# Optimization experiments

Hardware: AMD Instinct MI355X
Metric: run time of the kernel (lower is better)

## Reference

```python
import jax, jax.numpy as jnp
import numpy as np

LMDA = 1.0
SMOOTH = 1e-05

# 13 directional offsets (dz, dy, dx) matching the original slice pairs 1..13
OFFSETS = [
    (1, 0, 0), (0, 1, 0), (0, 0, 1),
    (1, 1, 0), (1, -1, 0),
    (0, 1, 1), (0, 1, -1),
    (1, 0, -1), (1, 0, 1),
    (1, -1, -1), (1, 1, -1),
    (-1, -1, -1), (-1, 1, -1),
]


def _shifted_diff(x, off):
    """x[..., pos-shift] - x[..., neg-shift] for offset off over last 3 dims."""
    sl_pos = tuple(slice(1, None) if o == 1 else (slice(None, -1) if o == -1 else slice(None)) for o in off)
    sl_neg = tuple(slice(None, -1) if o == 1 else (slice(1, None) if o == -1 else slice(None)) for o in off)
    return x[(Ellipsis,) + sl_pos] - x[(Ellipsis,) + sl_neg]


def setup_inputs() -> dict:
    key = jax.random.key(0)
    k1, k2 = jax.random.split(key)
    shape = (4, 1, 128, 192, 192)
    eps = 1e-6
    inp = jax.random.uniform(k1, shape, dtype=jnp.float32, minval=eps, maxval=1.0 - eps)
    tgt = jax.random.uniform(k2, shape, dtype=jnp.float32, minval=0.0, maxval=1.0)
    return {"input": inp, "target": tgt}


def reference(input, target):
    # region term: BCE with mean reduction
    bce = -jnp.mean(target * jnp.log(input) + (1.0 - target) * jnp.log(1.0 - input))

    # boundary term: 13 directional diff-product ratios
    acc = jnp.float32(0.0)
    for off in OFFSETS:
        di = _shifted_diff(input, off)
        dt = _shifted_diff(target, off)
        acc = acc + jnp.sum(di * dt) / (jnp.sum(dt * dt) + SMOOTH)
    boundary = 1.0 - acc / 13.0

    return LMDA * bce + boundary
```

## Files before the change

### kernel.cpp

```cpp
#include <hip/hip_runtime.h>
#include <math.h>

#define DX 192
#define DY 192
#define DZ 128
#define DB 4
#define DXY (DX*DY)
#define NTOT (DB*DZ*DXY)
#define XV (DX/4)
#define NCOL (DB*DZ*XV)
#define SEG 12
#define NSEG (DY/SEG)


__device__ inline float wred(float v) {
    #pragma unroll
    for (int o = 32; o > 0; o >>= 1) v += __shfl_down(v, o, 64);
    return v;
}

__device__ inline float4 ld4(const float* p) { return *(const float4*)p; }

#define TN(k, A1, A0, D1, D0) do { float di_=(A1)-(A0); float dt_=(D1)-(D0); \
    sk[k] += di_*dt_; rk[k] += dt_*dt_; } while(0)
#define TM(k, A1, A0, D1, D0) do { float di_=(A1)-(A0); float dt_=(D1)-(D0); \
    float dm_=fx3*dt_; sk[k] += di_*dm_; rk[k] += dt_*dm_; } while(0)
#define BCEACC(A0, D0) do { bces += (D0)*__logf(A0) + (1.0f-(D0))*__logf(1.0f-(A0)); } while(0)


#define ELEM_FULL(a0,a1,a2,a3,a4,a5,a6,a7, d0,d1,d2,d3,d4,d5,d6,d7) do { \
    TN(0,a4,a0,d4,d0); TN(1,a2,a0,d2,d0); TN(2,a1,a0,d1,d0); TN(3,a6,a0,d6,d0); \
    TN(4,a4,a2,d4,d2); TN(5,a3,a0,d3,d0); TN(6,a2,a1,d2,d1); TN(7,a4,a1,d4,d1); \
    TN(8,a5,a0,d5,d0); TN(9,a4,a3,d4,d3); TN(10,a6,a1,d6,d1); TN(11,a7,a0,d7,d0); \
    TN(12,a5,a2,d5,d2); BCEACC(a0,d0); } while(0)

#define ELEM_FX(a0,a1,a2,a3,a4,a5,a6,a7, d0,d1,d2,d3,d4,d5,d6,d7) do { \
    TN(0,a4,a0,d4,d0); TN(1,a2,a0,d2,d0); TM(2,a1,a0,d1,d0); TN(3,a6,a0,d6,d0); \
    TN(4,a4,a2,d4,d2); TM(5,a3,a0,d3,d0); TM(6,a2,a1,d2,d1); TM(7,a4,a1,d4,d1); \
    TM(8,a5,a0,d5,d0); TM(9,a4,a3,d4,d3); TM(10,a6,a1,d6,d1); TM(11,a7,a0,d7,d0); \
    TM(12,a5,a2,d5,d2); BCEACC(a0,d0); } while(0)

#define PEL_FULL(a0,a1,a4,a5, d0,d1,d4,d5) do { \
    TN(0,a4,a0,d4,d0); TN(2,a1,a0,d1,d0); TN(7,a4,a1,d4,d1); TN(8,a5,a0,d5,d0); \
    BCEACC(a0,d0); } while(0)
#define PEL_FX(a0,a1,a4,a5, d0,d1,d4,d5) do { \
    TN(0,a4,a0,d4,d0); TM(2,a1,a0,d1,d0); TM(7,a4,a1,d4,d1); TM(8,a5,a0,d5,d0); \
    BCEACC(a0,d0); } while(0)

#define ZEL_FULL(a0,a1,a2,a3, d0,d1,d2,d3) do { \
    TN(1,a2,a0,d2,d0); TN(2,a1,a0,d1,d0); TN(5,a3,a0,d3,d0); TN(6,a2,a1,d2,d1); \
    BCEACC(a0,d0); } while(0)
#define ZEL_FX(a0,a1,a2,a3, d0,d1,d2,d3) do { \
    TN(1,a2,a0,d2,d0); TM(2,a1,a0,d1,d0); TM(5,a3,a0,d3,d0); TM(6,a2,a1,d2,d1); \
    BCEACC(a0,d0); } while(0)

#define ZPEL_FULL(a0,a1, d0,d1) do { TN(2,a1,a0,d1,d0); BCEACC(a0,d0); } while(0)
#define ZPEL_FX(a0,a1, d0,d1)   do { TM(2,a1,a0,d1,d0); BCEACC(a0,d0); } while(0)

__global__ __launch_bounds__(256) void gc3d_main(const float* __restrict__ inp,
                                                 const float* __restrict__ tgt,
                                                 double* __restrict__ acc) {
    float sk[13] = {0,0,0,0,0,0,0,0,0,0,0,0,0};
    float rk[13] = {0,0,0,0,0,0,0,0,0,0,0,0,0};
    float bces = 0.f;

    int c   = blockIdx.x * 256 + threadIdx.x;
    int s   = blockIdx.y;
    int xv4 = c % XV;
    int zb  = c / XV;
    int z   = zb & (DZ - 1);
    int y0  = s * SEG;
    bool xlast = (xv4 == XV - 1);
    int   xe   = xlast ? 3 : 4;
    float fx3  = xlast ? 0.f : 1.f;
    bool lastseg = (s == NSEG - 1);
    int  nfull   = SEG - (lastseg ? 1 : 0);

    int base = (zb * DY + y0) * DX + xv4 * 4;
    const float* ip = inp + base;
    const float* tp = tgt + base;

    if (z != DZ - 1) {
        const float* ipz = ip + DXY;
        const float* tpz = tp + DXY;
        float4 i0 = ld4(ip),  i1 = ld4(ipz);
        float4 t0 = ld4(tp),  t1 = ld4(tpz);
        float i0e = ip[xe],  i1e = ipz[xe];
        float t0e = tp[xe],  t1e = tpz[xe];

        for (int it = 0; it < nfull; ++it) {
            ip += DX; ipz += DX; tp += DX; tpz += DX;
            float4 j0 = ld4(ip),  j1 = ld4(ipz);
            float4 u0 = ld4(tp),  u1 = ld4(tpz);
            float j0e = ip[xe],  j1e = ipz[xe];
            float u0e = tp[xe],  u1e = tpz[xe];

            ELEM_FULL(i0.x,i0.y, j0.x,j0.y, i1.x,i1.y, j1.x,j1.y,
                      t0.x,t0.y, u0.x,u0.y, t1.x,t1.y, u1.x,u1.y);
            ELEM_FULL(i0.y,i0.z, j0.y,j0.z, i1.y,i1.z, j1.y,j1.z,
                      t0.y,t0.z, u0.y,u0.z, t1.y,t1.z, u1.y,u1.z);
            ELEM_FULL(i0.z,i0.w, j0.z,j0.w, i1.z,i1.w, j1.z,j1.w,
                      t0.z,t0.w, u0.z,u0.w, t1.z,t1.w, u1.z,u1.w);
            ELEM_FX  (i0.w,i0e,  j0.w,j0e,  i1.w,i1e,  j1.w,j1e,
                      t0.w,t0e,  u0.w,u0e,  t1.w,t1e,  u1.w,u1e);

            i0 = j0; i1 = j1; t0 = u0; t1 = u1;
            i0e = j0e; i1e = j1e; t0e = u0e; t1e = u1e;
        }
        if (lastseg) {
            PEL_FULL(i0.x,i0.y, i1.x,i1.y, t0.x,t0.y, t1.x,t1.y);
            PEL_FULL(i0.y,i0.z, i1.y,i1.z, t0.y,t0.z, t1.y,t1.z);
            PEL_FULL(i0.z,i0.w, i1.z,i1.w, t0.z,t0.w, t1.z,t1.w);
            PEL_FX  (i0.w,i0e,  i1.w,i1e,  t0.w,t0e,  t1.w,t1e);
        }
    } else {
        float4 i0 = ld4(ip);
        float4 t0 = ld4(tp);
        float i0e = ip[xe];
        float t0e = tp[xe];

        for (int it = 0; it < nfull; ++it) {
            ip += DX; tp += DX;
            float4 j0 = ld4(ip);
            float4 u0 = ld4(tp);
            float j0e = ip[xe];
            float u0e = tp[xe];

            ZEL_FULL(i0.x,i0.y, j0.x,j0.y, t0.x,t0.y, u0.x,u0.y);
            ZEL_FULL(i0.y,i0.z, j0.y,j0.z, t0.y,t0.z, u0.y,u0.z);
            ZEL_FULL(i0.z,i0.w, j0.z,j0.w, t0.z,t0.w, u0.z,u0.w);
            ZEL_FX  (i0.w,i0e,  j0.w,j0e,  t0.w,t0e,  u0.w,u0e);

            i0 = j0; t0 = u0; i0e = j0e; t0e = u0e;
        }
        if (lastseg) {
            ZPEL_FULL(i0.x,i0.y, t0.x,t0.y);
            ZPEL_FULL(i0.y,i0.z, t0.y,t0.z);
            ZPEL_FULL(i0.z,i0.w, t0.z,t0.w);
            ZPEL_FX  (i0.w,i0e,  t0.w,t0e);
        }
    }

    float vals[27];
    #pragma unroll
    for (int q = 0; q < 13; q++) { vals[q] = sk[q]; vals[13 + q] = rk[q]; }
    vals[26] = bces;
    #pragma unroll
    for (int q = 0; q < 27; q++) vals[q] = wred(vals[q]);

    __shared__ float red[4][27];
    int lane = threadIdx.x & 63;
    int wave = threadIdx.x >> 6;
    if (lane == 0) {
        #pragma unroll
        for (int q = 0; q < 27; q++) red[wave][q] = vals[q];
    }
    __syncthreads();
    if (threadIdx.x < 27) {
        float t = red[0][threadIdx.x] + red[1][threadIdx.x]
                + red[2][threadIdx.x] + red[3][threadIdx.x];
        atomicAdd(&acc[threadIdx.x], (double)t);
    }
}

__global__ void gc3d_final(const double* __restrict__ acc, float* __restrict__ out) {
    if (threadIdx.x == 0 && blockIdx.x == 0) {
        double s = 0.0;
        #pragma unroll
        for (int k = 0; k < 13; k++) s += acc[k] / (acc[13 + k] + 1e-5);
        double bce = -acc[26] / (double)NTOT;
        out[0] = (float)(bce + 1.0 - s / 13.0);
    }
}

extern "C" void kernel_launch(void* const* d_in, const int* in_sizes, int n_in,
                              void* d_out, int out_size, void* d_ws, size_t ws_size,
                              hipStream_t stream) {
    const float* inp = (const float*)d_in[0];
    const float* tgt = (const float*)d_in[1];
    double* acc = (double*)d_ws;

    hipMemsetAsync(d_ws, 0, 27 * sizeof(double), stream);
    dim3 grid(NCOL / 256, NSEG);
    gc3d_main<<<grid, 256, 0, stream>>>(inp, tgt, acc);
    gc3d_final<<<1, 64, 0, stream>>>(acc, (float*)d_out);
}
```

Measured before the change: 231.5 us.

## Software-pipeline row loads with four rotating register sets and occupancy hint

The y-direction sweep is restructured into a manually unrolled loop that rotates four register sets, so loads for later rows are issued while the current row pair is being computed. The z-edge path likewise prefetches one row ahead with explicit register rotation and an unroll of two. Row addressing switches from pointer increments to base offsets. A min-blocks-per-CU launch bound is added to cap register use. The aim is to hide global load latency, at the cost of more live registers, which could cause spills under the tighter bound.

After: 571.6 us. 147% more time.

```diff
diff --git a/kernel.cpp b/kernel.cpp
--- a/kernel.cpp
+++ b/kernel.cpp
@@ -57,9 +57,43 @@
 #define ZPEL_FULL(a0,a1, d0,d1) do { TN(2,a1,a0,d1,d0); BCEACC(a0,d0); } while(0)
 #define ZPEL_FX(a0,a1, d0,d1)   do { TM(2,a1,a0,d1,d0); BCEACC(a0,d0); } while(0)
 
-__global__ __launch_bounds__(256) void gc3d_main(const float* __restrict__ inp,
-                                                 const float* __restrict__ tgt,
-                                                 double* __restrict__ acc) {
+#define DECLSET(S) float4 S##i0, S##i1, S##t0, S##t1; \
+                   float  S##ie, S##iz, S##te, S##tz;
+
+#define LOADSET(S, k) do { \
+    S##i0 = ld4(inp + off  + (k)*DX); S##i1 = ld4(inp + offz + (k)*DX); \
+    S##t0 = ld4(tgt + off  + (k)*DX); S##t1 = ld4(tgt + offz + (k)*DX); \
+    S##ie = inp[offe  + (k)*DX];      S##iz = inp[offze + (k)*DX]; \
+    S##te = tgt[offe  + (k)*DX];      S##tz = tgt[offze + (k)*DX]; } while(0)
+
+#define COMP(A,B) do { \
+    ELEM_FULL(A##i0.x,A##i0.y, B##i0.x,B##i0.y, A##i1.x,A##i1.y, B##i1.x,B##i1.y, \
+              A##t0.x,A##t0.y, B##t0.x,B##t0.y, A##t1.x,A##t1.y, B##t1.x,B##t1.y); \
+    ELEM_FULL(A##i0.y,A##i0.z, B##i0.y,B##i0.z, A##i1.y,A##i1.z, B##i1.y,B##i1.z, \
+              A##t0.y,A##t0.z, B##t0.y,B##t0.z, A##t1.y,A##t1.z, B##t1.y,B##t1.z); \
+    ELEM_FULL(A##i0.z,A##i0.w, B##i0.z,B##i0.w, A##i1.z,A##i1.w, B##i1.z,B##i1.w, \
+              A##t0.z,A##t0.w, B##t0.z,B##t0.w, A##t1.z,A##t1.w, B##t1.z,B##t1.w); \
+    ELEM_FX  (A##i0.w,A##ie,  B##i0.w,B##ie,  A##i1.w,A##iz,  B##i1.w,B##iz, \
+              A##t0.w,A##te,  B##t0.w,B##te,  A##t1.w,A##tz,  B##t1.w,B##tz); \
+    } while(0)
+
+#define PEELSET(S) do { \
+    PEL_FULL(S##i0.x,S##i0.y, S##i1.x,S##i1.y, S##t0.x,S##t0.y, S##t1.x,S##t1.y); \
+    PEL_FULL(S##i0.y,S##i0.z, S##i1.y,S##i1.z, S##t0.y,S##t0.z, S##t1.y,S##t1.z); \
+    PEL_FULL(S##i0.z,S##i0.w, S##i1.z,S##i1.w, S##t0.z,S##t0.w, S##t1.z,S##t1.w); \
+    PEL_FX  (S##i0.w,S##ie,  S##i1.w,S##iz,  S##t0.w,S##te,  S##t1.w,S##tz); \
+    } while(0)
+
+#define ZCOMP(A,B) do { \
+    ZEL_FULL(A##i0.x,A##i0.y, B##i0.x,B##i0.y, A##t0.x,A##t0.y, B##t0.x,B##t0.y); \
+    ZEL_FULL(A##i0.y,A##i0.z, B##i0.y,B##i0.z, A##t0.y,A##t0.z, B##t0.y,B##t0.z); \
+    ZEL_FULL(A##i0.z,A##i0.w, B##i0.z,B##i0.w, A##t0.z,A##t0.w, B##t0.z,B##t0.w); \
+    ZEL_FX  (A##i0.w,A##ie,  B##i0.w,B##ie,  A##t0.w,A##te,  B##t0.w,B##te); \
+    } while(0)
+
+__global__ __launch_bounds__(256, 4) void gc3d_main(const float* __restrict__ inp,
+                                                    const float* __restrict__ tgt,
+                                                    double* __restrict__ acc) {
     float sk[13] = {0,0,0,0,0,0,0,0,0,0,0,0,0};
     float rk[13] = {0,0,0,0,0,0,0,0,0,0,0,0,0};
     float bces = 0.f;
@@ -76,68 +110,57 @@
     bool lastseg = (s == NSEG - 1);
     int  nfull   = SEG - (lastseg ? 1 : 0);
 
-    int base = (zb * DY + y0) * DX + xv4 * 4;
-    const float* ip = inp + base;
-    const float* tp = tgt + base;
+    int off  = (zb * DY + y0) * DX + xv4 * 4;
+    int offe = off + xe;
+    int offz = off + DXY;
+    int offze = offz + xe;
 
     if (z != DZ - 1) {
-        const float* ipz = ip + DXY;
-        const float* tpz = tp + DXY;
-        float4 i0 = ld4(ip),  i1 = ld4(ipz);
-        float4 t0 = ld4(tp),  t1 = ld4(tpz);
-        float i0e = ip[xe],  i1e = ipz[xe];
-        float t0e = tp[xe],  t1e = tpz[xe];
-
-        for (int it = 0; it < nfull; ++it) {
-            ip += DX; ipz += DX; tp += DX; tpz += DX;
-            float4 j0 = ld4(ip),  j1 = ld4(ipz);
-            float4 u0 = ld4(tp),  u1 = ld4(tpz);
-            float j0e = ip[xe],  j1e = ipz[xe];
-            float u0e = tp[xe],  u1e = tpz[xe];
-
-            ELEM_FULL(i0.x,i0.y, j0.x,j0.y, i1.x,i1.y, j1.x,j1.y,
-                      t0.x,t0.y, u0.x,u0.y, t1.x,t1.y, u1.x,u1.y);
-            ELEM_FULL(i0.y,i0.z, j0.y,j0.z, i1.y,i1.z, j1.y,j1.z,
-                      t0.y,t0.z, u0.y,u0.z, t1.y,t1.z, u1.y,u1.z);
-            ELEM_FULL(i0.z,i0.w, j0.z,j0.w, i1.z,i1.w, j1.z,j1.w,
-                      t0.z,t0.w, u0.z,u0.w, t1.z,t1.w, u1.z,u1.w);
-            ELEM_FX  (i0.w,i0e,  j0.w,j0e,  i1.w,i1e,  j1.w,j1e,
-                      t0.w,t0e,  u0.w,u0e,  t1.w,t1e,  u1.w,u1e);
-
-            i0 = j0; i1 = j1; t0 = u0; t1 = u1;
-            i0e = j0e; i1e = j1e; t0e = u0e; t1e = u1e;
-        }
+        DECLSET(A) DECLSET(B) DECLSET(C) DECLSET(D)
+        LOADSET(A, 0); LOADSET(B, 1); LOADSET(C, 2);
+
+        for (int r = 0; r + 6 <= nfull; r += 4) {
+            LOADSET(D, 3); COMP(A, B);
+            LOADSET(A, 4); COMP(B, C);
+            LOADSET(B, 5); COMP(C, D);
+            LOADSET(C, 6); COMP(D, A);
+            off += 4 * DX; offz += 4 * DX; offe += 4 * DX; offze += 4 * DX;
+        }
+        LOADSET(D, 3);
+        COMP(A, B);
+        if (!lastseg) {
+            LOADSET(A, 4);
+            COMP(B, C);
+            COMP(C, D);
+            COMP(D, A);
+        } else {
+            COMP(B, C);
+            COMP(C, D);
+            PEELSET(D);
+        }
+    } else {
+        float4 Pi0 = ld4(inp + off),      Pt0 = ld4(tgt + off);
+        float  Pie = inp[offe],           Pte = tgt[offe];
+        float4 Qi0 = ld4(inp + off + DX), Qt0 = ld4(tgt + off + DX);
+        float  Qie = inp[offe + DX],      Qte = tgt[offe + DX];
+
+        #pragma unroll 2
+        for (int it = 0; it < nfull - 1; ++it) {
+            float4 Ri0 = ld4(inp + off + 2*DX), Rt0 = ld4(tgt + off + 2*DX);
+            float  Rie = inp[offe + 2*DX],      Rte = tgt[offe + 2*DX];
+
+            ZCOMP(P, Q);
+
+            Pi0 = Qi0; Pt0 = Qt0; Pie = Qie; Pte = Qte;
+            Qi0 = Ri0; Qt0 = Rt0; Qie = Rie; Qte = Rte;
+            off += DX; offe += DX;
+        }
+        ZCOMP(P, Q);
         if (lastseg) {
-            PEL_FULL(i0.x,i0.y, i1.x,i1.y, t0.x,t0.y, t1.x,t1.y);
-            PEL_FULL(i0.y,i0.z, i1.y,i1.z, t0.y,t0.z, t1.y,t1.z);
-            PEL_FULL(i0.z,i0.w, i1.z,i1.w, t0.z,t0.w, t1.z,t1.w);
-            PEL_FX  (i0.w,i0e,  i1.w,i1e,  t0.w,t0e,  t1.w,t1e);
-        }
-    } else {
-        float4 i0 = ld4(ip);
-        float4 t0 = ld4(tp);
-        float i0e = ip[xe];
-        float t0e = tp[xe];
-
-        for (int it = 0; it < nfull; ++it) {
-            ip += DX; tp += DX;
-            float4 j0 = ld4(ip);
-            float4 u0 = ld4(tp);
-            float j0e = ip[xe];
-            float u0e = tp[xe];
-
-            ZEL_FULL(i0.x,i0.y, j0.x,j0.y, t0.x,t0.y, u0.x,u0.y);
-            ZEL_FULL(i0.y,i0.z, j0.y,j0.z, t0.y,t0.z, u0.y,u0.z);
-            ZEL_FULL(i0.z,i0.w, j0.z,j0.w, t0.z,t0.w, u0.z,u0.w);
-            ZEL_FX  (i0.w,i0e,  j0.w,j0e,  t0.w,t0e,  u0.w,u0e);
-
-            i0 = j0; t0 = u0; i0e = j0e; t0e = u0e;
-        }
-        if (lastseg) {
-            ZPEL_FULL(i0.x,i0.y, t0.x,t0.y);
-            ZPEL_FULL(i0.y,i0.z, t0.y,t0.z);
-            ZPEL_FULL(i0.z,i0.w, t0.z,t0.w);
-            ZPEL_FX  (i0.w,i0e,  t0.w,t0e);
+            ZPEL_FULL(Qi0.x,Qi0.y, Qt0.x,Qt0.y);
+            ZPEL_FULL(Qi0.y,Qi0.z, Qt0.y,Qt0.z);
+            ZPEL_FULL(Qi0.z,Qi0.w, Qt0.z,Qt0.w);
+            ZPEL_FX  (Qi0.w,Qie,  Qt0.w,Qte);
         }
     }
 
```
